# Optimization experiments

Measured on AMD Instinct MI355X. Metric: run time of the kernel, lower is better.

The kernel has to match this reference:

```python
import jax, jax.numpy as jnp
import numpy as np

N_NODES = 10000
N_EDGES = 80000
F_IN = 128
H1 = 2048
H2 = 2048
H3 = 1024


def _sgconv(x, pos, src, dst, W_in, b_in, W_out, b_out):
    # geo-GCN SpatialGraphConv with hidden_size=1:
    # message(j->i) = relu(Linear(pos_j - pos_i)) * x_j ; aggr='add' ; then Linear out
    rel = pos[src] - pos[dst]                      # [E, 2]  (pos_j - pos_i)
    scale = jax.nn.relu(rel @ W_in + b_in)         # [E, C_in]
    msg = scale * x[src]                           # [E, C_in]
    agg = jax.ops.segment_sum(msg, dst, num_segments=x.shape[0])  # [N, C_in]
    return agg @ W_out + b_out                     # [N, C_out]


def setup_inputs() -> dict:
    key = jax.random.key(0)
    ks = jax.random.split(key, 12)
    x = jax.random.normal(ks[0], (N_NODES, F_IN), dtype=jnp.float32)
    pos = jax.random.normal(ks[1], (N_NODES, 2), dtype=jnp.float32)
    edge_index = jax.random.randint(ks[2], (2, N_EDGES), 0, N_NODES, dtype=jnp.int32)

    def lin(k, fan_in, fan_out):
        lim = 1.0 / np.sqrt(fan_in)
        kw, kb = jax.random.split(k)
        W = jax.random.uniform(kw, (fan_in, fan_out), jnp.float32, -lim, lim)
        b = jax.random.uniform(kb, (fan_out,), jnp.float32, -lim, lim)
        return W, b

    W_in1, b_in1 = lin(ks[3], 2, F_IN)
    W_out1, b_out1 = lin(ks[4], F_IN, H1)
    W_in2, b_in2 = lin(ks[5], 2, H1)
    W_out2, b_out2 = lin(ks[6], H1, H2)
    W_in3, b_in3 = lin(ks[7], 2, H2)
    W_out3, b_out3 = lin(ks[8], H2, H3)

    return {
        "x": x, "pos": pos, "edge_index": edge_index,
        "W_in1": W_in1, "b_in1": b_in1, "W_out1": W_out1, "b_out1": b_out1,
        "W_in2": W_in2, "b_in2": b_in2, "W_out2": W_out2, "b_out2": b_out2,
        "W_in3": W_in3, "b_in3": b_in3, "W_out3": W_out3, "b_out3": b_out3,
    }


def reference(x, pos, edge_index,
              W_in1, b_in1, W_out1, b_out1,
              W_in2, b_in2, W_out2, b_out2,
              W_in3, b_in3, W_out3, b_out3):
    src, dst = edge_index[0], edge_index[1]  # flow source_to_target: j=src, i=dst
    h = jax.nn.relu(_sgconv(x, pos, src, dst, W_in1, b_in1, W_out1, b_out1))
    h = jax.nn.relu(_sgconv(h, pos, src, dst, W_in2, b_in2, W_out2, b_out2))
    h = jax.nn.relu(_sgconv(h, pos, src, dst, W_in3, b_in3, W_out3, b_out3))
    # F.normalize(h, dim=1): L2 normalize rows with eps clamp 1e-12
    norm = jnp.linalg.norm(h, axis=1, keepdims=True)
    return h / jnp.maximum(norm, 1e-12)
```

## Files before the change

kernel.cpp:

```cpp
#include <hip/hip_runtime.h>
#include <hip/hip_bf16.h>

#define DEVI __device__ __forceinline__

constexpr int NN = 10000;
constexpr int NE = 80000;
constexpr int AGG_ROWS = 10240;
constexpr int ES_CAP = 110016;

typedef __attribute__((ext_vector_type(8))) short bf16x8;
typedef __attribute__((ext_vector_type(4))) float f32x4;

DEVI float blo(unsigned int u) {
  union { unsigned int i; float f; } c; c.i = u << 16; return c.f;
}
DEVI float bhi(unsigned int u) {
  union { unsigned int i; float f; } c; c.i = u & 0xffff0000u; return c.f;
}
DEVI unsigned short f2b(float f) {
  union { float f; unsigned int i; } c; c.f = f;
  unsigned int i = c.i;
  return (unsigned short)((i + 0x7fffu + ((i >> 16) & 1u)) >> 16);
}
DEVI void st1(float* p, float v) { *p = v; }
DEVI void st1(unsigned short* p, float v) { *p = f2b(v); }
DEVI void store8b(unsigned short* p, const float v[8]) {
  int4 pk;
  pk.x = (int)((unsigned)f2b(v[0]) | ((unsigned)f2b(v[1]) << 16));
  pk.y = (int)((unsigned)f2b(v[2]) | ((unsigned)f2b(v[3]) << 16));
  pk.z = (int)((unsigned)f2b(v[4]) | ((unsigned)f2b(v[5]) << 16));
  pk.w = (int)((unsigned)f2b(v[6]) | ((unsigned)f2b(v[7]) << 16));
  *reinterpret_cast<int4*>(p) = pk;
}

DEVI void gload16(const void* g, void* l) {
  __builtin_amdgcn_global_load_lds(
      (const __attribute__((address_space(1))) void*)g,
      (__attribute__((address_space(3))) void*)l, 16, 0, 0);
}

__global__ __launch_bounds__(256)
void hist_kernel(const int* __restrict__ dst, int* __restrict__ cnt) {
  int e = blockIdx.x * 256 + threadIdx.x;
  if (e < NE) atomicAdd(&cnt[dst[e]], 1);
}

__global__ __launch_bounds__(1024)
void scan_kernel(const int* __restrict__ cnt, int* __restrict__ off,
                 int* __restrict__ cursor) {
  __shared__ int wpart[16];
  __shared__ int carry;
  int tid = threadIdx.x, lane = tid & 63, w = tid >> 6;
  if (tid == 0) carry = 0;
  __syncthreads();
  for (int base = 0; base < NN; base += 1024) {
    int i = base + tid;
    int v = (i < NN) ? ((cnt[i] + 3) & ~3) : 0;
    int s = v;
#pragma unroll
    for (int o = 1; o < 64; o <<= 1) { int t = __shfl_up(s, o); if (lane >= o) s += t; }
    if (lane == 63) wpart[w] = s;
    __syncthreads();
    if (w == 0) {
      int ws = (lane < 16) ? wpart[lane] : 0;
#pragma unroll
      for (int o = 1; o < 16; o <<= 1) { int t = __shfl_up(ws, o); if (lane >= o) ws += t; }
      if (lane < 16) wpart[lane] = ws;
    }
    __syncthreads();
    int ex = carry + (w ? wpart[w - 1] : 0) + s - v;
    if (i < NN) { off[i] = ex; cursor[i] = ex; }
    __syncthreads();
    if (tid == 0) carry += wpart[15];
    __syncthreads();
  }
}

__global__ __launch_bounds__(256)
void bucket_kernel(const int* __restrict__ src, const int* __restrict__ dst,
                   const float* __restrict__ pos,
                   int* __restrict__ cursor, int* __restrict__ es,
                   float* __restrict__ rel) {
  int e = blockIdx.x * 256 + threadIdx.x;
  if (e < NE) {
    int s = src[e], d = dst[e];
    int p = atomicAdd(&cursor[d], 1);
    float2 ps = *reinterpret_cast<const float2*>(pos + 2 * s);
    float2 pd = *reinterpret_cast<const float2*>(pos + 2 * d);
    es[p] = s;
    *reinterpret_cast<float2*>(rel + 2 * p) = make_float2(ps.x - pd.x, ps.y - pd.y);
  }
}

__global__ __launch_bounds__(256)
void transpose_w(const float* __restrict__ W, unsigned short* __restrict__ WT,
                 int K, int N) {
  __shared__ float tile[32][33];
  int tx = threadIdx.x & 31, ty = threadIdx.x >> 5;
  int n0 = blockIdx.x * 32, k0 = blockIdx.y * 32;
#pragma unroll
  for (int j = 0; j < 32; j += 8)
    tile[ty + j][tx] = W[(size_t)(k0 + ty + j) * N + n0 + tx];
  __syncthreads();
#pragma unroll
  for (int j = 0; j < 32; j += 8)
    WT[(size_t)(n0 + ty + j) * K + k0 + tx] = f2b(tile[tx][ty + j]);
}

__global__ __launch_bounds__(256)
void gather_l1(const float* __restrict__ x,
               const int* __restrict__ off, const int* __restrict__ cnt,
               const int* __restrict__ es, const float* __restrict__ rel,
               const float* __restrict__ Win, const float* __restrict__ bin,
               unsigned short* __restrict__ agg) {
  constexpr int C = 128;
  int lane = threadIdx.x & 63;
  int i = blockIdx.x * 4 + (threadIdx.x >> 6);
  if (i >= NN) return;
  int c = lane * 2;
  float w00 = Win[c], w01 = Win[c + 1];
  float w10 = Win[C + c], w11 = Win[C + c + 1];
  float b0 = bin[c], b1 = bin[c + 1];
  float a0 = 0.f, a1 = 0.f;
  int s0 = off[i], n = cnt[i];

  for (int k = 0; k < n; k += 4) {
    int4 s4 = *reinterpret_cast<const int4*>(es + s0 + k);
    float4 ra = *reinterpret_cast<const float4*>(rel + 2 * (s0 + k));
    float4 rb = *reinterpret_cast<const float4*>(rel + 2 * (s0 + k) + 4);
    float2 q0 = *reinterpret_cast<const float2*>(x + (size_t)s4.x * C + c);
    float2 q1 = *reinterpret_cast<const float2*>(x + (size_t)s4.y * C + c);
    float2 q2 = *reinterpret_cast<const float2*>(x + (size_t)s4.z * C + c);
    float2 q3 = *reinterpret_cast<const float2*>(x + (size_t)s4.w * C + c);
    {
      float sc0 = fmaxf(fmaf(ra.x, w00, fmaf(ra.y, w10, b0)), 0.f);
      float sc1 = fmaxf(fmaf(ra.x, w01, fmaf(ra.y, w11, b1)), 0.f);
      a0 = fmaf(sc0, q0.x, a0); a1 = fmaf(sc1, q0.y, a1);
    }
    if (k + 1 < n) {
      float sc0 = fmaxf(fmaf(ra.z, w00, fmaf(ra.w, w10, b0)), 0.f);
      float sc1 = fmaxf(fmaf(ra.z, w01, fmaf(ra.w, w11, b1)), 0.f);
      a0 = fmaf(sc0, q1.x, a0); a1 = fmaf(sc1, q1.y, a1);
    }
    if (k + 2 < n) {
      float sc0 = fmaxf(fmaf(rb.x, w00, fmaf(rb.y, w10, b0)), 0.f);
      float sc1 = fmaxf(fmaf(rb.x, w01, fmaf(rb.y, w11, b1)), 0.f);
      a0 = fmaf(sc0, q2.x, a0); a1 = fmaf(sc1, q2.y, a1);
    }
    if (k + 3 < n) {
      float sc0 = fmaxf(fmaf(rb.z, w00, fmaf(rb.w, w10, b0)), 0.f);
      float sc1 = fmaxf(fmaf(rb.z, w01, fmaf(rb.w, w11, b1)), 0.f);
      a0 = fmaf(sc0, q3.x, a0); a1 = fmaf(sc1, q3.y, a1);
    }
  }
  unsigned int pk = (unsigned)f2b(a0) | ((unsigned)f2b(a1) << 16);
  *reinterpret_cast<unsigned int*>(agg + (size_t)i * C + c) = pk;
}

__global__ __launch_bounds__(256)
void gather_chunk(const unsigned short* __restrict__ x,
                  const int* __restrict__ off, const int* __restrict__ cnt,
                  const int* __restrict__ es, const float* __restrict__ rel,
                  const float* __restrict__ Win, const float* __restrict__ bin,
                  unsigned short* __restrict__ agg, int ngb8) {
  constexpr int C = 2048;
  constexpr int V = 8;
  int wgid = blockIdx.x;
  int half = wgid >= ngb8;
  int base = half ? wgid - ngb8 : wgid;
  int chunk = (base & 7) + (half << 3);
  int grp = base >> 3;
  int lane = threadIdx.x & 63;
  int wid = threadIdx.x >> 6;
  int slot = lane >> 4;
  int l16 = lane & 15;
  int i = grp * 16 + wid * 4 + slot;
  int c = chunk * 128 + l16 * V;

  float w0[V], w1[V], bb[V], acc[V];
#pragma unroll
  for (int j = 0; j < V; ++j) {
    w0[j] = Win[c + j]; w1[j] = Win[C + c + j]; bb[j] = bin[c + j]; acc[j] = 0.f;
  }
  int s0 = off[i], n = cnt[i];

  auto fma8 = [&](float rx, float ry, const int4& q) {
    float xv[V] = { blo(q.x), bhi(q.x), blo(q.y), bhi(q.y),
                    blo(q.z), bhi(q.z), blo(q.w), bhi(q.w) };
#pragma unroll
    for (int j = 0; j < V; ++j) {
      float sc = fmaxf(fmaf(rx, w0[j], fmaf(ry, w1[j], bb[j])), 0.f);
      acc[j] = fmaf(sc, xv[j], acc[j]);
    }
  };
  for (int k = 0; k < n; k += 4) {
    int4 s4 = *reinterpret_cast<const int4*>(es + s0 + k);
    float4 ra = *reinterpret_cast<const float4*>(rel + 2 * (s0 + k));
    float4 rb = *reinterpret_cast<const float4*>(rel + 2 * (s0 + k) + 4);
    int4 q0 = *reinterpret_cast<const int4*>(x + (size_t)s4.x * C + c);
    int4 q1 = *reinterpret_cast<const int4*>(x + (size_t)s4.y * C + c);
    int4 q2 = *reinterpret_cast<const int4*>(x + (size_t)s4.z * C + c);
    int4 q3 = *reinterpret_cast<const int4*>(x + (size_t)s4.w * C + c);
    fma8(ra.x, ra.y, q0);
    if (k + 1 < n) fma8(ra.z, ra.w, q1);
    if (k + 2 < n) fma8(rb.x, rb.y, q2);
    if (k + 3 < n) fma8(rb.z, rb.w, q3);
  }
  store8b(agg + (size_t)i * C + c, acc);
}

template <typename OT>
__global__ __launch_bounds__(512, 4)
void gemm320(const unsigned short* __restrict__ A,
             const unsigned short* __restrict__ BT,
             const float* __restrict__ bias, OT* __restrict__ out,
             int M, int N, int K) {
  __shared__ unsigned short lds[2 * 14336];
  const int t = threadIdx.x;
  const int lane = t & 63, wid = t >> 6;
  const int wr = wid >> 1, wc = wid & 1;

  const int nwg = gridDim.x * gridDim.y;
  const int orig = blockIdx.y * gridDim.x + blockIdx.x;
  const int swz = (orig & 7) * (nwg >> 3) + (orig >> 3);
  const int bx = swz % gridDim.x, by = swz / gridDim.x;
  const int m0 = by * 320, n0 = bx * 128;
  const int nk = K >> 5;

  const int lrow = lane >> 2;
  const int schunk = (lane & 3) ^ ((lrow >> 1) & 3);
  const bool isA = wid < 4;
  const int aw = wid & 3;
  const unsigned short* gSrc = isA
      ? A + (size_t)(m0 + aw * 80 + lrow) * K + schunk * 8
      : BT + (size_t)(n0 + aw * 32 + lrow) * K + schunk * 8;
  const int lBase = isA ? (aw * 5 * 512 + lane * 8)
                        : (10240 + aw * 2 * 512 + lane * 8);

  auto STAGE = [&](int buf, int kt) {
    const unsigned short* g = gSrc + kt * 32;
    unsigned short* l = lds + buf * 14336 + lBase;
    if (isA) {
#pragma unroll
      for (int jj = 0; jj < 5; ++jj)
        gload16(g + (size_t)(jj * 16) * K, l + jj * 512);
    } else {
#pragma unroll
      for (int jj = 0; jj < 2; ++jj)
        gload16(g + (size_t)(jj * 16) * K, l + jj * 512);
    }
  };

  const int frow = lane & 15;
  const int fslot = ((lane >> 4) ^ ((frow >> 1) & 3)) * 8;
  const int paOff = (wr * 80 + frow) * 32 + fslot;
  const int pbOff = 10240 + (wc * 64 + frow) * 32 + fslot;

  f32x4 acc[5][4];
#pragma unroll
  for (int m = 0; m < 5; ++m)
#pragma unroll
    for (int n = 0; n < 4; ++n) acc[m][n] = 0.f;

  STAGE(0, 0);

  int cur = 0;
  for (int kt = 0; kt < nk; ++kt) {
    if (kt + 1 < nk) {
      STAGE(cur ^ 1, kt + 1);
      if (isA) asm volatile("s_waitcnt vmcnt(5)" ::: "memory");
      else     asm volatile("s_waitcnt vmcnt(2)" ::: "memory");
    } else {
      asm volatile("s_waitcnt vmcnt(0)" ::: "memory");
    }
    asm volatile("s_barrier" ::: "memory");
    const unsigned short* pa = lds + cur * 14336 + paOff;
    const unsigned short* pb = lds + cur * 14336 + pbOff;
    bf16x8 bf[4];
#pragma unroll
    for (int n = 0; n < 4; ++n)
      bf[n] = *reinterpret_cast<const bf16x8*>(pb + n * 512);
    __builtin_amdgcn_s_setprio(1);
#pragma unroll
    for (int m = 0; m < 5; ++m) {
      bf16x8 af = *reinterpret_cast<const bf16x8*>(pa + m * 512);
#pragma unroll
      for (int n = 0; n < 4; ++n)
        acc[m][n] = __builtin_amdgcn_mfma_f32_16x16x32_bf16(
            af, bf[n], acc[m][n], 0, 0, 0);
    }
    __builtin_amdgcn_s_setprio(0);
    asm volatile("s_barrier" ::: "memory");
    cur ^= 1;
  }

  const int ccol = lane & 15;
  const int crow = (lane >> 4) * 4;
  float bv[4];
#pragma unroll
  for (int n = 0; n < 4; ++n)
    bv[n] = bias[n0 + wc * 64 + n * 16 + ccol];
#pragma unroll
  for (int m = 0; m < 5; ++m) {
    int gm0 = m0 + wr * 80 + m * 16 + crow;
#pragma unroll
    for (int r = 0; r < 4; ++r) {
      int gm = gm0 + r;
      if (gm < M) {
        size_t base = (size_t)gm * N + n0 + wc * 64 + ccol;
#pragma unroll
        for (int n = 0; n < 4; ++n)
          st1(out + base + n * 16, fmaxf(acc[m][n][r] + bv[n], 0.f));
      }
    }
  }
}

__global__ __launch_bounds__(256)
void l2norm_kernel(float* __restrict__ out) {
  constexpr int C = 1024;
  float* p = out + (size_t)blockIdx.x * C;
  float4 v = *reinterpret_cast<const float4*>(p + threadIdx.x * 4);
  float s = v.x * v.x + v.y * v.y + v.z * v.z + v.w * v.w;
#pragma unroll
  for (int o = 32; o > 0; o >>= 1) s += __shfl_down(s, o);
  __shared__ float wsum[4];
  if ((threadIdx.x & 63) == 0) wsum[threadIdx.x >> 6] = s;
  __syncthreads();
  float tot = wsum[0] + wsum[1] + wsum[2] + wsum[3];
  float inv = 1.0f / fmaxf(sqrtf(tot), 1e-12f);
  float4 r = make_float4(v.x * inv, v.y * inv, v.z * inv, v.w * inv);
  *reinterpret_cast<float4*>(p + threadIdx.x * 4) = r;
}

extern "C" void kernel_launch(void* const* d_in, const int* in_sizes, int n_in,
                              void* d_out, int out_size, void* d_ws, size_t ws_size,
                              hipStream_t stream) {
  (void)in_sizes; (void)n_in; (void)out_size; (void)ws_size;
  const float* x     = (const float*)d_in[0];
  const float* pos   = (const float*)d_in[1];
  const int*   ei    = (const int*)d_in[2];
  const int*   srcv  = ei;
  const int*   dstv  = ei + NE;
  const float* Win1  = (const float*)d_in[3];
  const float* bin1  = (const float*)d_in[4];
  const float* Wout1 = (const float*)d_in[5];
  const float* bout1 = (const float*)d_in[6];
  const float* Win2  = (const float*)d_in[7];
  const float* bin2  = (const float*)d_in[8];
  const float* Wout2 = (const float*)d_in[9];
  const float* bout2 = (const float*)d_in[10];
  const float* Win3  = (const float*)d_in[11];
  const float* bin3  = (const float*)d_in[12];
  const float* Wout3 = (const float*)d_in[13];
  const float* bout3 = (const float*)d_in[14];
  float* outp = (float*)d_out;

  char* ws = (char*)d_ws;
  unsigned short* aggb = (unsigned short*)ws;
  unsigned short* h1   = (unsigned short*)(ws + 41943040);
  unsigned short* W2T  = (unsigned short*)(ws + 82903040);
  unsigned short* W3T  = (unsigned short*)(ws + 91291648);
  unsigned short* W1T  = (unsigned short*)(ws + 95485952);
  int* cnt    = (int*)(ws + 96010240);
  int* off    = (int*)(ws + 96050240);
  int* cursor = (int*)(ws + 96090240);
  int* es     = (int*)(ws + 96130240);
  float* rel  = (float*)(ws + 96570304);
  unsigned short* h2 = (unsigned short*)d_out;

  const dim3 blk(256);
  const int eb = (NE + 255) / 256;
  const int ngb8 = ((NN + 15) / 16) * 8;

  hipMemsetAsync(cnt, 0, NN * sizeof(int), stream);
  hipMemsetAsync(es, 0, ES_CAP * sizeof(int), stream);
  hist_kernel<<<eb, blk, 0, stream>>>(dstv, cnt);
  scan_kernel<<<1, 1024, 0, stream>>>(cnt, off, cursor);
  bucket_kernel<<<eb, blk, 0, stream>>>(srcv, dstv, pos, cursor, es, rel);

  transpose_w<<<dim3(2048 / 32, 128 / 32),  blk, 0, stream>>>(Wout1, W1T, 128, 2048);
  transpose_w<<<dim3(2048 / 32, 2048 / 32), blk, 0, stream>>>(Wout2, W2T, 2048, 2048);
  transpose_w<<<dim3(1024 / 32, 2048 / 32), blk, 0, stream>>>(Wout3, W3T, 2048, 1024);

  hipMemsetAsync(aggb + (size_t)NN * 2048, 0, (size_t)(AGG_ROWS - NN) * 2048 * 2, stream);

  gather_l1<<<(NN + 3) / 4, blk, 0, stream>>>(x, off, cnt, es, rel, Win1, bin1, aggb);
  gemm320<unsigned short><<<dim3(2048 / 128, AGG_ROWS / 320), 512, 0, stream>>>(
      aggb, W1T, bout1, h1, NN, 2048, 128);

  gather_chunk<<<2 * ngb8, blk, 0, stream>>>(h1, off, cnt, es, rel, Win2, bin2, aggb, ngb8);
  gemm320<unsigned short><<<dim3(2048 / 128, AGG_ROWS / 320), 512, 0, stream>>>(
      aggb, W2T, bout2, h2, NN, 2048, 2048);

  gather_chunk<<<2 * ngb8, blk, 0, stream>>>(h2, off, cnt, es, rel, Win3, bin3, aggb, ngb8);
  gemm320<float><<<dim3(1024 / 128, AGG_ROWS / 320), 512, 0, stream>>>(
      aggb, W3T, bout3, outp, NN, 1024, 2048);

  l2norm_kernel<<<NN, blk, 0, stream>>>(outp);
}
```

Baseline: 317.5 us.

## Add 160x128-tile GEMM with BK=64 for layer-3 output projection

Adds a new gemm160 kernel using 256-thread blocks, 160x128 output tiles, K-step of 64 with double-buffered dynamic LDS and XOR-swizzled layout, and launches it for the third layer's 2048->1024 projection instead of gemm320. With N=1024 the old 320-row tiling produced only 8x32 blocks; smaller M tiles double the block count to improve CU occupancy and load balance. It trades some per-block operand reuse for more parallelism, and relies on a larger dynamic shared-memory allocation.

```diff
diff --git a/kernel.cpp b/kernel.cpp
--- a/kernel.cpp
+++ b/kernel.cpp
@@ -290,6 +290,112 @@
             af, bf[n], acc[m][n], 0, 0, 0);
     }
     __builtin_amdgcn_s_setprio(0);
+    asm volatile("s_barrier" ::: "memory");
+    cur ^= 1;
+  }
+
+  const int ccol = lane & 15;
+  const int crow = (lane >> 4) * 4;
+  float bv[4];
+#pragma unroll
+  for (int n = 0; n < 4; ++n)
+    bv[n] = bias[n0 + wc * 64 + n * 16 + ccol];
+#pragma unroll
+  for (int m = 0; m < 5; ++m) {
+    int gm0 = m0 + wr * 80 + m * 16 + crow;
+#pragma unroll
+    for (int r = 0; r < 4; ++r) {
+      int gm = gm0 + r;
+      if (gm < M) {
+        size_t base = (size_t)gm * N + n0 + wc * 64 + ccol;
+#pragma unroll
+        for (int n = 0; n < 4; ++n)
+          st1(out + base + n * 16, fmaxf(acc[m][n][r] + bv[n], 0.f));
+      }
+    }
+  }
+}
+
+template <typename OT>
+__global__ __launch_bounds__(256, 2)
+void gemm160(const unsigned short* __restrict__ A,
+             const unsigned short* __restrict__ BT,
+             const float* __restrict__ bias, OT* __restrict__ out,
+             int M, int N, int K) {
+  extern __shared__ unsigned short lds[];
+  const int t = threadIdx.x;
+  const int lane = t & 63, wid = t >> 6;
+  const int wr = wid >> 1, wc = wid & 1;
+
+  const int nwg = gridDim.x * gridDim.y;
+  const int orig = blockIdx.y * gridDim.x + blockIdx.x;
+  const int swz = (orig & 7) * (nwg >> 3) + (orig >> 3);
+  const int bx = swz % gridDim.x, by = swz / gridDim.x;
+  const int m0 = by * 160, n0 = bx * 128;
+  const int nk = K >> 6;
+
+  const int lrow = lane >> 3;
+  const int schunk = (lane & 7) ^ lrow;
+  const unsigned short* gA = A + (size_t)(m0 + wid * 40 + lrow) * K + schunk * 8;
+  const unsigned short* gB = BT + (size_t)(n0 + wid * 32 + lrow) * K + schunk * 8;
+  unsigned short* lA = lds + (wid * 5) * 512 + lane * 8;
+  unsigned short* lB = lds + 20480 + (wid * 4) * 512 + lane * 8;
+
+  auto STAGE = [&](int buf, int kt) {
+    const size_t ko = (size_t)kt << 6;
+#pragma unroll
+    for (int jj = 0; jj < 5; ++jj)
+      gload16(gA + (size_t)(jj * 8) * K + ko, lA + buf * 10240 + jj * 512);
+#pragma unroll
+    for (int jj = 0; jj < 4; ++jj)
+      gload16(gB + (size_t)(jj * 8) * K + ko, lB + buf * 8192 + jj * 512);
+  };
+
+  const int frow = lane & 15;
+  const int fr7 = frow & 7;
+  const int slot0 = ((lane >> 4) ^ fr7) * 8;
+  const int slot1 = ((4 + (lane >> 4)) ^ fr7) * 8;
+  const int paRow = (wr * 80 + frow) * 64;
+  const int pbRow = (wc * 64 + frow) * 64;
+
+  f32x4 acc[5][4];
+#pragma unroll
+  for (int m = 0; m < 5; ++m)
+#pragma unroll
+    for (int n = 0; n < 4; ++n) acc[m][n] = 0.f;
+
+  STAGE(0, 0);
+
+  int cur = 0;
+  for (int kt = 0; kt < nk; ++kt) {
+    if (kt + 1 < nk) {
+      STAGE(cur ^ 1, kt + 1);
+      asm volatile("s_waitcnt vmcnt(9)" ::: "memory");
+    } else {
+      asm volatile("s_waitcnt vmcnt(0)" ::: "memory");
+    }
+    asm volatile("s_barrier" ::: "memory");
+    const unsigned short* pa = lds + cur * 10240 + paRow;
+    const unsigned short* pb = lds + 20480 + cur * 8192 + pbRow;
+#pragma unroll
+    for (int ks = 0; ks < 2; ++ks) {
+      const int sl = ks ? slot1 : slot0;
+      bf16x8 af[5], bf[4];
+#pragma unroll
+      for (int m = 0; m < 5; ++m)
+        af[m] = *reinterpret_cast<const bf16x8*>(pa + m * 1024 + sl);
+#pragma unroll
+      for (int n = 0; n < 4; ++n)
+        bf[n] = *reinterpret_cast<const bf16x8*>(pb + n * 1024 + sl);
+      __builtin_amdgcn_s_setprio(1);
+#pragma unroll
+      for (int m = 0; m < 5; ++m)
+#pragma unroll
+        for (int n = 0; n < 4; ++n)
+          acc[m][n] = __builtin_amdgcn_mfma_f32_16x16x32_bf16(
+              af[m], bf[n], acc[m][n], 0, 0, 0);
+      __builtin_amdgcn_s_setprio(0);
+    }
     asm volatile("s_barrier" ::: "memory");
     cur ^= 1;
   }
@@ -369,6 +475,9 @@
   float* rel  = (float*)(ws + 96570304);
   unsigned short* h2 = (unsigned short*)d_out;
 
+  hipFuncSetAttribute((const void*)gemm160<float>,
+                      hipFuncAttributeMaxDynamicSharedMemorySize, 73728);
+
   const dim3 blk(256);
   const int eb = (NE + 255) / 256;
   const int ngb8 = ((NN + 15) / 16) * 8;
@@ -394,7 +503,7 @@
       aggb, W2T, bout2, h2, NN, 2048, 2048);
 
   gather_chunk<<<2 * ngb8, blk, 0, stream>>>(h2, off, cnt, es, rel, Win3, bin3, aggb, ngb8);
-  gemm320<float><<<dim3(1024 / 128, AGG_ROWS / 320), 512, 0, stream>>>(
+  gemm160<float><<<dim3(1024 / 128, AGG_ROWS / 160), blk, 73728, stream>>>(
       aggb, W3T, bout3, outp, NN, 1024, 2048);
 
   l2norm_kernel<<<NN, blk, 0, stream>>>(outp);
```

Result: no change. 311.9 us (-1.8%).
